# Kernel optimization log

Measured on AMD Instinct MI355X. Metric: run time of the kernel, lower is better.

The kernel has to match this reference:

```python
import jax, jax.numpy as jnp
import numpy as np

B, C, DET, T = 16, 1, 512, 180  # batch, channels, detector size (= image side, circle=True), n angles


def setup_inputs() -> dict:
    key = jax.random.key(0)
    x = jax.random.normal(key, (B, C, DET, T), dtype=jnp.float32)  # sinogram [B,C,det,theta]
    return {"x": x}


def _ramp_filter(x):
    """skimage-style ramp (Ram-Lak) filter along detector axis (axis=2)."""
    det = x.shape[2]
    size = max(64, int(2 ** np.ceil(np.log2(2 * det))))  # zero-padded FFT length
    n = np.concatenate([np.arange(1, size // 2 + 1, 2), np.arange(size // 2 - 1, 0, -2)])
    f = np.zeros(size, dtype=np.float64)
    f[0] = 0.25
    f[1::2] = -1.0 / (np.pi * n) ** 2
    fourier = (2.0 * np.real(np.fft.fft(f))).astype(np.float32)  # [size]
    xp = jnp.pad(x, ((0, 0), (0, 0), (0, size - det), (0, 0)))
    proj = jnp.fft.fft(xp, axis=2) * fourier[None, None, :, None]
    return jnp.real(jnp.fft.ifft(proj, axis=2))[:, :, :det, :].astype(x.dtype)


def _forward(x):
    b, c, det, n_theta = x.shape
    xf = _ramp_filter(x)
    # align_corners=False unit grid over the image (circle=True -> grid side == det)
    u = ((2.0 * jnp.arange(det, dtype=x.dtype) + 1.0) / det - 1.0)
    yg = u[:, None]  # [det,1] (meshgrid 'ij': Y varies over rows)
    xg = u[None, :]  # [1,det]
    rad = jnp.arange(n_theta, dtype=x.dtype) * jnp.asarray(np.pi / 180.0, x.dtype)
    cos_t, sin_t = jnp.cos(rad), jnp.sin(rad)

    # Note: the grid X coord theta_x[i]=(2i+1)/T-1 maps (align_corners=False) to pixel
    # index exactly i, so the width-axis bilinear interp reduces to taking angle column i.
    def body(reco, inp):
        i, c_, s_ = inp
        col = jax.lax.dynamic_index_in_dim(xf, i, axis=3, keepdims=False)  # [B,C,det]
        t = xg * c_ - yg * s_                      # [det,det] rotated coordinate
        iy = ((t + 1.0) * det - 1.0) / 2.0         # grid_sample align_corners=False
        i0f = jnp.floor(iy)
        w1 = iy - i0f
        w0 = 1.0 - w1
        i0 = i0f.astype(jnp.int32)
        i1 = i0 + 1
        m0 = ((i0 >= 0) & (i0 < det)).astype(xf.dtype)  # zeros padding
        m1 = ((i1 >= 0) & (i1 < det)).astype(xf.dtype)
        g0 = jnp.take(col, jnp.clip(i0, 0, det - 1), axis=2)  # [B,C,det,det]
        g1 = jnp.take(col, jnp.clip(i1, 0, det - 1), axis=2)
        return reco + (w0 * m0) * g0 + (w1 * m1) * g1, None

    reco0 = jnp.zeros((b, c, det, det), xf.dtype)
    reco, _ = jax.lax.scan(body, reco0, (jnp.arange(n_theta), cos_t, sin_t))

    # reconstruction circle mask (scikit=False -> radius^2 <= 1 - 1/in_size)
    mask = (xg ** 2 + yg ** 2) <= (1.0 - 1.0 / det)
    reco = jnp.where(mask[None, None], reco, jnp.zeros((), reco.dtype))
    return reco * jnp.asarray(np.pi / (2.0 * n_theta), reco.dtype)


def reference(x):
    return _forward(x)
```

## Files before the change

kernel.cpp:

```cpp
#include <hip/hip_runtime.h>
#include <math.h>

#define DET 512
#define NB  16
#define NT  180
#define PI_D 3.14159265358979323846
#define NPAIR 89
#define PADQ 108
#define NGP  45
#define PKI_ROW 1536
#define NUNIT 113

#define TT_OFF   8192
#define XF0_OFF  (TT_OFF + 512*512*2)
#define XF90_OFF (XF0_OFF + 32768)
#define PK_OFF   (XF90_OFF + 32768)

typedef _Float16 half8  __attribute__((ext_vector_type(8)));
typedef _Float16 half2v __attribute__((ext_vector_type(2)));
typedef float    float4v __attribute__((ext_vector_type(4)));

__device__ inline void fmix_lo(float& acc, float w, unsigned int pk) {
  asm("v_fma_mix_f32 %0, %1, %2, %0 op_sel_hi:[0,1,0]"
      : "+v"(acc) : "v"(w), "v"(pk));
}
__device__ inline void fmix_hi(float& acc, float w, unsigned int pk) {
  asm("v_fma_mix_f32 %0, %1, %2, %0 op_sel:[0,1,0] op_sel_hi:[0,1,0]"
      : "+v"(acc) : "v"(w), "v"(pk));
}

__global__ __launch_bounds__(256) void init_kernel(char* __restrict__ wsb) {
  int tid = threadIdx.x;
  int d = blockIdx.x;
  _Float16* tth = (_Float16*)(wsb + TT_OFF);
#pragma unroll
  for (int c = 0; c < 2; c++) {
    int k = tid * 2 + c;
    int delta = d - k;
    float w;
    if (delta == 0) w = 0.5f;
    else if (delta & 1) { double dd = (double)delta; w = (float)(-2.0 / (PI_D * PI_D * dd * dd)); }
    else w = 0.f;
    tth[(size_t)d * 512 + k] = (_Float16)(w * 1024.0f);
  }
  if (d == 0 && tid < NPAIR) {
    float2* trigp = (float2*)wsb;
    int t = tid + 1, u = 179 - tid;
    float rt = (float)t * (float)(PI_D / 180.0);
    float ru = (float)u * (float)(PI_D / 180.0);
    double ct = cos((double)rt), st = sin((double)rt);
    double cu = cos((double)ru), su = sin((double)ru);
    float2 cs;
    cs.x = (float)((ct - cu) * 0.5);
    cs.y = (float)((st + su) * 0.5);
    trigp[tid] = cs;
  }
}

__global__ __launch_bounds__(256) void filter_kernel(const float* __restrict__ x,
                                                     char* __restrict__ wsb) {
  __shared__ _Float16 xs_h[16][512];
  __shared__ _Float16 xs_l[16][512];
  __shared__ float xfs[16][65];
  const _Float16* tth = (const _Float16*)(wsb + TT_OFF);
  unsigned int* pkg = (unsigned int*)(wsb + PK_OFF);

  int tid = threadIdx.x;
  int p = blockIdx.x, b = blockIdx.y;
  int dt0 = blockIdx.z * 2;

  int m = tid & 15, kp = tid >> 4;
  int tS;
  if (p < 11) tS = (m < 8) ? (8 * p + 1 + m) : (164 - 8 * p + m);
  else        tS = (m == 0) ? 89 : ((m == 1) ? 91 : ((m == 3) ? 90 : 0));
  const float* xb = x + (size_t)b * DET * NT + tS;
#pragma unroll 8
  for (int pass = 0; pass < 16; pass++) {
    int k = pass * 32 + kp * 2;
    int c = k >> 3, h = k & 7;
    int phys = (((c ^ (m & 7)) << 3) | h);
    float v0 = xb[(size_t)k * NT];
    float v1 = xb[(size_t)(k + 1) * NT];
    _Float16 h0 = (_Float16)v0, h1 = (_Float16)v1;
    half2v hh = {h0, h1};
    half2v ll = {(_Float16)(v0 - (float)h0), (_Float16)(v1 - (float)h1)};
    *(half2v*)&xs_h[m][phys] = hh;
    *(half2v*)&xs_l[m][phys] = ll;
  }
  __syncthreads();

  int nprb = (p < 11) ? 8 : 1;
  int tpb0 = (p < 11) ? 8 * p : 88;
  if (blockIdx.z == 0) {
    int idx = (tid < 108) ? tid : (620 + (tid - 108));
    uint2 z2; z2.x = 0u; z2.y = 0u;
    for (int pr = 0; pr < nprb; pr++) {
      int tq = (p < 11) ? (tpb0 + pr) : 88;
      int gp = (tq <= 44) ? tq : 88 - tq;
      *(uint2*)&pkg[((size_t)b * NGP + gp) * PKI_ROW + 2 * idx] = z2;
    }
  }

  int lane = tid & 63, wv = tid >> 6;
  int mm = lane & 15, q = lane >> 4;
  const _Float16* arh = &xs_h[mm][0];
  const _Float16* arl = &xs_l[mm][0];
  int e = mm & 7;
  int mp = tid >> 5, cc = (tid & 31) * 2;
  int rT = (p < 11) ? mp : 0;
  int rU = (p < 11) ? (15 - mp) : 1;
  int tpp = (p < 11) ? (8 * p + mp) : 88;
  bool dopack = (p < 11) || (mp == 0);
  int gp_  = (tpp <= 44) ? tpp : 88 - tpp;
  int slot = (tpp <= 44) ? 0 : 1;

  for (int dti = 0; dti < 2; dti++) {
    int dt = dt0 + dti;
    int dw = dt * 64 + wv * 16 + mm;
    const _Float16* th = tth + (size_t)dw * 512;
    float4v acc0 = {0.f, 0.f, 0.f, 0.f};
    float4v acc1 = {0.f, 0.f, 0.f, 0.f};
#pragma unroll 4
    for (int kc = 0; kc < 512; kc += 32) {
      int ph = ((((kc >> 3) + q) ^ e) << 3);
      half8 Ah = *(const half8*)&arh[ph];
      half8 Al = *(const half8*)&arl[ph];
      half8 Bh = *(const half8*)&th[kc + q * 8];
      acc0 = __builtin_amdgcn_mfma_f32_16x16x32_f16(Ah, Bh, acc0, 0, 0, 0);
      acc1 = __builtin_amdgcn_mfma_f32_16x16x32_f16(Al, Bh, acc1, 0, 0, 0);
    }
    if (dti > 0) __syncthreads();
#pragma unroll
    for (int i = 0; i < 4; i++)
      xfs[q * 4 + i][wv * 16 + mm] = (acc0[i] + acc1[i]) * 0.0009765625f;
    __syncthreads();
    if (dopack) {
      float ft0 = xfs[rT][cc], ft1 = xfs[rT][cc + 1];
      float fu0 = xfs[rU][cc], fu1 = xfs[rU][cc + 1];
      auto p0 = __builtin_amdgcn_cvt_pkrtz(ft0, fu0);
      auto p1 = __builtin_amdgcn_cvt_pkrtz(ft1, fu1);
      unsigned int w0, w1;
      __builtin_memcpy(&w0, &p0, 4);
      __builtin_memcpy(&w1, &p1, 4);
      unsigned int* row = pkg + ((size_t)b * NGP + gp_) * PKI_ROW;
      int en = PADQ + dt * 64 + cc;
      row[2 * en + slot]     = w0;
      row[2 * en + 2 + slot] = w1;
      if (tpp == 44) {
        row[2 * en + 1] = w0;
        row[2 * en + 3] = w1;
      }
    }
    if (p == 11 && tid < 64) {
      float* f0  = (float*)(wsb + XF0_OFF)  + (size_t)b * DET;
      float* f90 = (float*)(wsb + XF90_OFF) + (size_t)b * DET;
      f0[dt * 64 + tid]  = xfs[2][tid];
      f90[dt * 64 + tid] = xfs[3][tid];
    }
  }
}

#define PROCESS(c_, s_, SW)                                                    \
  {                                                                            \
    float inner = fmaf(-(s_), q_, 363.5f);                                     \
    float iyA = fmaf( (c_), p_, inner);                                        \
    float iyB = fmaf(-(c_), p_, inner);                                        \
    int   iA = (int)iyA;  float wA = __builtin_amdgcn_fractf(iyA);             \
    int   iB = (int)iyB;  float wB = __builtin_amdgcn_fractf(iyB);             \
    float vA = 1.f - wA, vB = 1.f - wB;                                        \
    uint4 rA, rB, rMA, rMB;                                                    \
    __builtin_memcpy(&rA,  &colI[2 * iA], 16);                                 \
    __builtin_memcpy(&rB,  &colI[2 * iB], 16);                                 \
    __builtin_memcpy(&rMA, &colI[2 * (726 - iA)], 16);                         \
    __builtin_memcpy(&rMB, &colI[2 * (726 - iB)], 16);                         \
    unsigned tA0 = SW ? rA.y : rA.x,  tA1 = SW ? rA.w : rA.z;                  \
    unsigned uA0 = SW ? rA.x : rA.y,  uA1 = SW ? rA.z : rA.w;                  \
    unsigned tB0 = SW ? rB.y : rB.x,  tB1 = SW ? rB.w : rB.z;                  \
    unsigned uB0 = SW ? rB.x : rB.y,  uB1 = SW ? rB.z : rB.w;                  \
    unsigned tMA0 = SW ? rMA.y : rMA.x,  tMA1 = SW ? rMA.w : rMA.z;            \
    unsigned uMA0 = SW ? rMA.x : rMA.y,  uMA1 = SW ? rMA.z : rMA.w;            \
    unsigned tMB0 = SW ? rMB.y : rMB.x,  tMB1 = SW ? rMB.w : rMB.z;            \
    unsigned uMB0 = SW ? rMB.x : rMB.y,  uMB1 = SW ? rMB.z : rMB.w;            \
    fmix_lo(A1, vA, tA0);  fmix_lo(A1, wA, tA1);                               \
    fmix_hi(A1, vB, tB0);  fmix_hi(A1, wB, tB1);                               \
    fmix_lo(A2, vB, tB0);  fmix_lo(A2, wB, tB1);                               \
    fmix_hi(A2, vA, tA0);  fmix_hi(A2, wA, tA1);                               \
    fmix_lo(A3, wA, tMA0); fmix_lo(A3, vA, tMA1);                              \
    fmix_hi(A3, wB, tMB0); fmix_hi(A3, vB, tMB1);                              \
    fmix_lo(A4, wB, tMB0); fmix_lo(A4, vB, tMB1);                              \
    fmix_hi(A4, wA, tMA0); fmix_hi(A4, vA, tMA1);                              \
    if (doQ) {                                                                 \
      fmix_lo(B1, wA, uMA0); fmix_lo(B1, vA, uMA1);                            \
      fmix_hi(B1, vB, uB0);  fmix_hi(B1, wB, uB1);                             \
      fmix_lo(B2, wB, uMB0); fmix_lo(B2, vB, uMB1);                            \
      fmix_hi(B2, vA, uA0);  fmix_hi(B2, wA, uA1);                             \
      fmix_lo(B3, vA, uA0);  fmix_lo(B3, wA, uA1);                             \
      fmix_hi(B3, wB, uMB0); fmix_hi(B3, vB, uMB1);                            \
      fmix_lo(B4, vB, uB0);  fmix_lo(B4, wB, uB1);                             \
      fmix_hi(B4, wA, uMA0); fmix_hi(B4, vA, uMA1);                            \
    }                                                                          \
  }

__global__ __launch_bounds__(256, 8) void backproj_kernel(
    const char* __restrict__ wsb, float* __restrict__ out) {
  __shared__ unsigned int pk[2][PKI_ROW];
  int tid = threadIdx.x;
  int b   = blockIdx.y;
  int bx  = blockIdx.x;
  int lx = tid & 15, ly = tid >> 4;
  float* ob = out + (size_t)b * DET * DET;

  if (bx == NUNIT) {
    const int LDEAD[10] = {10,8,6,5,4,3,2,2,1,1};
    for (int a = 0; a < 10; a++)
      for (int bt = 0; bt < LDEAD[a]; bt++) {
        int X1 = 16*a + lx, X2 = 511 - X1;
        int Y1 = 16*bt + ly, Y2 = 511 - Y1;
        ob[(size_t)Y1*DET + X1] = 0.f;
        ob[(size_t)Y1*DET + X2] = 0.f;
        ob[(size_t)Y2*DET + X1] = 0.f;
        ob[(size_t)Y2*DET + X2] = 0.f;
      }
    return;
  }

  int a = (bx>=6)+(bx>=14)+(bx>=24)+(bx>=35)+(bx>=47)+(bx>=58)+(bx>=68)
        + (bx>=77)+(bx>=85)+(bx>=92)+(bx>=98)+(bx>=103)+(bx>=107)+(bx>=110)+(bx>=112);
  int Sa, bs;
  if (a < 8) { Sa = (int)((0x443A2F23180E0600ULL >> (8*a)) & 0xFF);
               bs = (int)((0x070605040506080AULL >> (8*a)) & 0xFF); }
  else       { Sa = (int)((0x706E6B67625C554DULL >> (8*(a-8))) & 0xFF);
               bs = (int)((0x0F0E0D0C0B0A0908ULL >> (8*(a-8))) & 0xFF); }
  int bt = bx - Sa + bs;
  bool doQ = (a != bt);
  int tx = 16*a, ty = 16*bt;

  int X1 = tx + lx, X2 = 511 - X1;
  int Y1 = ty + ly, Y2 = 511 - Y1;
  float p_ = (float)X1 - 255.5f;
  float q_ = (float)Y1 - 255.5f;

  int w = tid >> 6, l = tid & 63;
  int mkx = 481 - 32*a;
  int mky = 505 - 32*bt - 8*w;
  bool wlive = (mkx*mkx + mky*mky <= 261632);

  const float2* trigp = (const float2*)wsb;
  const unsigned int* pkg = (const unsigned int*)(wsb + PK_OFF) + (size_t)b * NGP * PKI_ROW;

  float A1=0.f, A2=0.f, A3=0.f, A4=0.f;
  float B1=0.f, B2=0.f, B3=0.f, B4=0.f;

  auto stage_group = [&](int g, int par) {
    {
      const unsigned int* src = pkg + (size_t)g * PKI_ROW + w * 256 + l * 4;
      char* dst = (char*)&pk[par][0] + w * 1024;
      __builtin_amdgcn_global_load_lds(
          (const __attribute__((address_space(1))) unsigned int*)src,
          (__attribute__((address_space(3))) unsigned int*)dst, 16, 0, 0);
    }
    if (w < 2) {
      const unsigned int* src = pkg + (size_t)g * PKI_ROW + (w + 4) * 256 + l * 4;
      char* dst = (char*)&pk[par][0] + (w + 4) * 1024;
      __builtin_amdgcn_global_load_lds(
          (const __attribute__((address_space(1))) unsigned int*)src,
          (__attribute__((address_space(3))) unsigned int*)dst, 16, 0, 0);
    }
  };

  stage_group(0, 0);
  __syncthreads();

  for (int g = 0; g < NGP; g++) {
    if (g + 1 < NGP) stage_group(g + 1, (g + 1) & 1);
    float2 cs = trigp[g];
    const unsigned int* colI = &pk[g & 1][0];
    if (wlive) {
      PROCESS(cs.x, cs.y, 0);
      if (g != 44) PROCESS(cs.y, cs.x, 1);
    }
    __syncthreads();
  }

  const float* f0  = (const float*)(wsb + XF0_OFF)  + (size_t)b * DET;
  const float* f90 = (const float*)(wsb + XF90_OFF) + (size_t)b * DET;
  const float SC = (float)(PI_D / 360.0);
  int kx = 2*X1 - 511, ky = 2*Y1 - 511;
  bool in = (kx*kx + ky*ky) <= 261632;

  float g0x1 = f0[X1], g0x2 = f0[X2];
  float g90y1 = f90[Y1], g90y2 = f90[Y2];
  float P1 = A1 + g0x1 + g90y2;
  float P2 = A2 + g0x2 + g90y2;
  float P3 = A3 + g0x2 + g90y1;
  float P4 = A4 + g0x1 + g90y1;
  ob[(size_t)Y1*DET + X1] = in ? P1*SC : 0.f;
  ob[(size_t)Y1*DET + X2] = in ? P2*SC : 0.f;
  ob[(size_t)Y2*DET + X2] = in ? P3*SC : 0.f;
  ob[(size_t)Y2*DET + X1] = in ? P4*SC : 0.f;

  if (doQ) {
    float g0y1 = f0[Y1], g0y2 = f0[Y2];
    float g90x1 = f90[X1], g90x2 = f90[X2];
    float Q1 = B1 + g0y1 + g90x2;
    float Q2 = B2 + g0y1 + g90x1;
    float Q3 = B3 + g0y2 + g90x1;
    float Q4 = B4 + g0y2 + g90x2;
    Q1 = in ? Q1*SC : 0.f;
    Q2 = in ? Q2*SC : 0.f;
    Q3 = in ? Q3*SC : 0.f;
    Q4 = in ? Q4*SC : 0.f;
    __syncthreads();
    float* qs = (float*)&pk[0][0];
    qs[(0*16 + lx)*17 + ly] = Q1;
    qs[(1*16 + lx)*17 + ly] = Q2;
    qs[(2*16 + lx)*17 + ly] = Q3;
    qs[(3*16 + lx)*17 + ly] = Q4;
    __syncthreads();
    float o1 = qs[(0*16 + ly)*17 + lx];
    float o2 = qs[(1*16 + ly)*17 + lx];
    float o3 = qs[(2*16 + ly)*17 + lx];
    float o4 = qs[(3*16 + ly)*17 + lx];
    int r1 = tx + ly, r2 = 511 - r1;
    int c1 = ty + lx, c2 = 511 - c1;
    ob[(size_t)r1*DET + c1] = o1;
    ob[(size_t)r2*DET + c1] = o2;
    ob[(size_t)r2*DET + c2] = o3;
    ob[(size_t)r1*DET + c2] = o4;
  }
}

extern "C" void kernel_launch(void* const* d_in, const int* in_sizes, int n_in,
                              void* d_out, int out_size, void* d_ws, size_t ws_size,
                              hipStream_t stream) {
  (void)in_sizes; (void)n_in; (void)out_size; (void)ws_size;
  const float* x = (const float*)d_in[0];
  float* out = (float*)d_out;
  char*  wsb = (char*)d_ws;

  init_kernel<<<512, 256, 0, stream>>>(wsb);
  filter_kernel<<<dim3(12, 16, 4), 256, 0, stream>>>(x, wsb);
  backproj_kernel<<<dim3(NUNIT + 1, 16), 256, 0, stream>>>(wsb, out);
}
```

Measured before the change: 153.9 us.

## Triple-buffer LDS projection staging with depth-2 prefetch and vmcnt-gated barriers

Staging of packed projection columns moves from double to triple buffering in LDS, prefetching two angle groups ahead. Each loop barrier now waits only for the group about to be consumed, via an explicit s_waitcnt vmcnt(6), instead of a full __syncthreads drain. Trig values are cached in shared memory, and the direct-to-LDS loads switch from 16-byte to six 4-byte loads per wave. The goal is to hide global latency behind the FMA work. The cost is more load instructions, more LDS per block, and reliance on an exact per-wave outstanding-load count.

After: 161.2 us. 4.7% more time.

```diff
diff --git a/kernel.cpp b/kernel.cpp
--- a/kernel.cpp
+++ b/kernel.cpp
@@ -159,6 +159,12 @@
     }
   }
 }
+
+#define PIPE_BARRIER(N)                                                        \
+  asm volatile("s_waitcnt vmcnt(" #N ") lgkmcnt(0)" ::: "memory");             \
+  __builtin_amdgcn_sched_barrier(0);                                           \
+  __builtin_amdgcn_s_barrier();                                                \
+  __builtin_amdgcn_sched_barrier(0);
 
 #define PROCESS(c_, s_, SW)                                                    \
   {                                                                            \
@@ -203,7 +209,8 @@
 
 __global__ __launch_bounds__(256, 8) void backproj_kernel(
     const char* __restrict__ wsb, float* __restrict__ out) {
-  __shared__ unsigned int pk[2][PKI_ROW];
+  __shared__ unsigned int pk[3][PKI_ROW];
+  __shared__ float2 trigs[NGP + 1];
   int tid = threadIdx.x;
   int b   = blockIdx.y;
   int bx  = blockIdx.x;
@@ -245,41 +252,39 @@
   int mky = 505 - 32*bt - 8*w;
   bool wlive = (mkx*mkx + mky*mky <= 261632);
 
-  const float2* trigp = (const float2*)wsb;
+  if (tid < NGP) trigs[tid] = ((const float2*)wsb)[tid];
+
   const unsigned int* pkg = (const unsigned int*)(wsb + PK_OFF) + (size_t)b * NGP * PKI_ROW;
 
   float A1=0.f, A2=0.f, A3=0.f, A4=0.f;
   float B1=0.f, B2=0.f, B3=0.f, B4=0.f;
 
-  auto stage_group = [&](int g, int par) {
-    {
-      const unsigned int* src = pkg + (size_t)g * PKI_ROW + w * 256 + l * 4;
-      char* dst = (char*)&pk[par][0] + w * 1024;
+  auto stage_group = [&](int g) {
+    const char* srcb = (const char*)(pkg + (size_t)g * PKI_ROW);
+    char* dstb = (char*)&pk[g % 3][0];
+#pragma unroll
+    for (int i = 0; i < 6; i++) {
+      int c = w * 6 + i;
       __builtin_amdgcn_global_load_lds(
-          (const __attribute__((address_space(1))) unsigned int*)src,
-          (__attribute__((address_space(3))) unsigned int*)dst, 16, 0, 0);
-    }
-    if (w < 2) {
-      const unsigned int* src = pkg + (size_t)g * PKI_ROW + (w + 4) * 256 + l * 4;
-      char* dst = (char*)&pk[par][0] + (w + 4) * 1024;
-      __builtin_amdgcn_global_load_lds(
-          (const __attribute__((address_space(1))) unsigned int*)src,
-          (__attribute__((address_space(3))) unsigned int*)dst, 16, 0, 0);
+          (const __attribute__((address_space(1))) unsigned int*)(srcb + c * 256 + l * 4),
+          (__attribute__((address_space(3))) unsigned int*)(dstb + c * 256),
+          4, 0, 0);
     }
   };
 
-  stage_group(0, 0);
+  stage_group(0);
+  stage_group(1);
   __syncthreads();
 
   for (int g = 0; g < NGP; g++) {
-    if (g + 1 < NGP) stage_group(g + 1, (g + 1) & 1);
-    float2 cs = trigp[g];
-    const unsigned int* colI = &pk[g & 1][0];
+    if (g + 2 < NGP) stage_group(g + 2);
+    float2 cs = trigs[g];
+    const unsigned int* colI = &pk[g % 3][0];
     if (wlive) {
       PROCESS(cs.x, cs.y, 0);
       if (g != 44) PROCESS(cs.y, cs.x, 1);
     }
-    __syncthreads();
+    if (g + 2 < NGP) { PIPE_BARRIER(6) } else { PIPE_BARRIER(0) }
   }
 
   const float* f0  = (const float*)(wsb + XF0_OFF)  + (size_t)b * DET;
```

## Drop init kernel; build filter weights in LDS and trig per block

Applied to the files above, without the earlier changes.

Removes the separate init launch that wrote the Toeplitz ramp-filter matrix and trig table to workspace. The filter kernel now builds a compact 8-row shifted copy of the Toeplitz weights in shared memory and reads its B operands from LDS instead of global memory. The backprojection kernel computes its cos/sin table per block in shared memory. This saves one kernel launch and the global traffic for the weight matrix, at the cost of redundant per-block setup. The old trig table stored averaged cos/sin pairs for angles t and 180-t, while the new one stores plain cos/sin of angle t, with float instead of double precision.

After: 142.1 us. 7.7% less time.

```diff
diff --git a/kernel.cpp b/kernel.cpp
--- a/kernel.cpp
+++ b/kernel.cpp
@@ -17,6 +17,7 @@
 #define PK_OFF   (XF90_OFF + 32768)
 
 typedef _Float16 half8  __attribute__((ext_vector_type(8)));
+typedef _Float16 half4v __attribute__((ext_vector_type(4)));
 typedef _Float16 half2v __attribute__((ext_vector_type(2)));
 typedef float    float4v __attribute__((ext_vector_type(4)));
 
@@ -27,34 +28,6 @@
 __device__ inline void fmix_hi(float& acc, float w, unsigned int pk) {
   asm("v_fma_mix_f32 %0, %1, %2, %0 op_sel:[0,1,0] op_sel_hi:[0,1,0]"
       : "+v"(acc) : "v"(w), "v"(pk));
-}
-
-__global__ __launch_bounds__(256) void init_kernel(char* __restrict__ wsb) {
-  int tid = threadIdx.x;
-  int d = blockIdx.x;
-  _Float16* tth = (_Float16*)(wsb + TT_OFF);
-#pragma unroll
-  for (int c = 0; c < 2; c++) {
-    int k = tid * 2 + c;
-    int delta = d - k;
-    float w;
-    if (delta == 0) w = 0.5f;
-    else if (delta & 1) { double dd = (double)delta; w = (float)(-2.0 / (PI_D * PI_D * dd * dd)); }
-    else w = 0.f;
-    tth[(size_t)d * 512 + k] = (_Float16)(w * 1024.0f);
-  }
-  if (d == 0 && tid < NPAIR) {
-    float2* trigp = (float2*)wsb;
-    int t = tid + 1, u = 179 - tid;
-    float rt = (float)t * (float)(PI_D / 180.0);
-    float ru = (float)u * (float)(PI_D / 180.0);
-    double ct = cos((double)rt), st = sin((double)rt);
-    double cu = cos((double)ru), su = sin((double)ru);
-    float2 cs;
-    cs.x = (float)((ct - cu) * 0.5);
-    cs.y = (float)((st + su) * 0.5);
-    trigp[tid] = cs;
-  }
 }
 
 __global__ __launch_bounds__(256) void filter_kernel(const float* __restrict__ x,
@@ -62,12 +35,31 @@
   __shared__ _Float16 xs_h[16][512];
   __shared__ _Float16 xs_l[16][512];
   __shared__ float xfs[16][65];
-  const _Float16* tth = (const _Float16*)(wsb + TT_OFF);
+  __shared__ _Float16 wls[8][1032];
   unsigned int* pkg = (unsigned int*)(wsb + PK_OFF);
 
   int tid = threadIdx.x;
   int p = blockIdx.x, b = blockIdx.y;
   int dt0 = blockIdx.z * 2;
+
+  {
+    int k0 = tid * 4;
+    const float CSC = (float)(-2048.0 / (PI_D * PI_D));
+#pragma unroll
+    for (int r = 0; r < 8; r++) {
+      half4v v;
+#pragma unroll
+      for (int j = 0; j < 4; j++) {
+        int delta = 511 - (k0 + j) - r;
+        float wv;
+        if (delta == 0) wv = 512.0f;
+        else if (delta & 1) wv = CSC / (float)(delta * delta);
+        else wv = 0.0f;
+        v[j] = (_Float16)wv;
+      }
+      *(half4v*)&wls[r][k0] = v;
+    }
+  }
 
   int m = tid & 15, kp = tid >> 4;
   int tS;
@@ -117,7 +109,8 @@
   for (int dti = 0; dti < 2; dti++) {
     int dt = dt0 + dti;
     int dw = dt * 64 + wv * 16 + mm;
-    const _Float16* th = tth + (size_t)dw * 512;
+    int sdw = 511 - dw;
+    const _Float16* thl = &wls[sdw & 7][sdw & ~7];
     float4v acc0 = {0.f, 0.f, 0.f, 0.f};
     float4v acc1 = {0.f, 0.f, 0.f, 0.f};
 #pragma unroll 4
@@ -125,7 +118,7 @@
       int ph = ((((kc >> 3) + q) ^ e) << 3);
       half8 Ah = *(const half8*)&arh[ph];
       half8 Al = *(const half8*)&arl[ph];
-      half8 Bh = *(const half8*)&th[kc + q * 8];
+      half8 Bh = *(const half8*)&thl[kc + q * 8];
       acc0 = __builtin_amdgcn_mfma_f32_16x16x32_f16(Ah, Bh, acc0, 0, 0, 0);
       acc1 = __builtin_amdgcn_mfma_f32_16x16x32_f16(Al, Bh, acc1, 0, 0, 0);
     }
@@ -204,6 +197,7 @@
 __global__ __launch_bounds__(256, 8) void backproj_kernel(
     const char* __restrict__ wsb, float* __restrict__ out) {
   __shared__ unsigned int pk[2][PKI_ROW];
+  __shared__ float2 trigs[48];
   int tid = threadIdx.x;
   int b   = blockIdx.y;
   int bx  = blockIdx.x;
@@ -245,7 +239,12 @@
   int mky = 505 - 32*bt - 8*w;
   bool wlive = (mkx*mkx + mky*mky <= 261632);
 
-  const float2* trigp = (const float2*)wsb;
+  if (tid < NGP) {
+    float th = (float)(tid + 1) * (float)(PI_D / 180.0);
+    float2 cs; cs.x = cosf(th); cs.y = sinf(th);
+    trigs[tid] = cs;
+  }
+
   const unsigned int* pkg = (const unsigned int*)(wsb + PK_OFF) + (size_t)b * NGP * PKI_ROW;
 
   float A1=0.f, A2=0.f, A3=0.f, A4=0.f;
@@ -273,7 +272,7 @@
 
   for (int g = 0; g < NGP; g++) {
     if (g + 1 < NGP) stage_group(g + 1, (g + 1) & 1);
-    float2 cs = trigp[g];
+    float2 cs = trigs[g];
     const unsigned int* colI = &pk[g & 1][0];
     if (wlive) {
       PROCESS(cs.x, cs.y, 0);
@@ -338,7 +337,6 @@
   float* out = (float*)d_out;
   char*  wsb = (char*)d_ws;
 
-  init_kernel<<<512, 256, 0, stream>>>(wsb);
   filter_kernel<<<dim3(12, 16, 4), 256, 0, stream>>>(x, wsb);
   backproj_kernel<<<dim3(NUNIT + 1, 16), 256, 0, stream>>>(wsb, out);
 }
```
